# Kernel optimization log

Measured on AMD Instinct MI355X. Metric: run time of the kernel, lower is better.

Reference implementation:

```python
import jax, jax.numpy as jnp
import numpy as np
import math

B, N, E, H = 2, 10000, 160000, 128
ET = 8
EPS = 1e-5


def setup_inputs() -> dict:
    key = jax.random.key(0)
    ks = jax.random.split(key, 20)
    s = 1.0 / math.sqrt(H)
    inp = {
        "hidden": jax.random.normal(ks[0], (B, N, H), jnp.float32),
        "time_emb": jax.random.normal(ks[1], (B, N, H), jnp.float32),
        "edge_index": jax.random.randint(ks[2], (2, E), 0, N),
        "edge_type": jax.random.randint(ks[3], (E,), 0, ET),
        # parameters
        "edge_emb": jax.random.normal(ks[4], (ET, H), jnp.float32),
        "Wq": jax.random.normal(ks[5], (H, H), jnp.float32) * s,
        "bq": jnp.zeros((H,), jnp.float32),
        "Wk": jax.random.normal(ks[6], (H, H), jnp.float32) * s,
        "bk": jnp.zeros((H,), jnp.float32),
        "Wv": jax.random.normal(ks[7], (H, H), jnp.float32) * s,
        "bv": jnp.zeros((H,), jnp.float32),
        "We": jax.random.normal(ks[8], (H, 1), jnp.float32) * s,
        "be": jnp.zeros((1,), jnp.float32),
        "W1": jax.random.normal(ks[9], (3 * H, H), jnp.float32) * (1.0 / math.sqrt(3 * H)),
        "b1": jnp.zeros((H,), jnp.float32),
        "W2": jax.random.normal(ks[10], (H, H), jnp.float32) * s,
        "b2": jnp.zeros((H,), jnp.float32),
        "gamma": jnp.ones((H,), jnp.float32),
        "beta": jnp.zeros((H,), jnp.float32),
    }
    return inp


def _forward(hidden, time_emb, edge_index, edge_type, edge_emb,
             Wq, bq, Wk, bk, Wv, bv, We, be, W1, b1, W2, b2, gamma, beta):
    src, tgt = edge_index[0], edge_index[1]
    # edge-wise gathers: [B, E, H]
    src_h = hidden[:, src]
    tgt_h = hidden[:, tgt]
    src_t = time_emb[:, src]
    tgt_t = time_emb[:, tgt]
    edge_h = edge_emb[edge_type][None, :, :]  # [1, E, H] broadcasts over batch

    query = (tgt_h + tgt_t) @ Wq + bq
    key = (src_h + src_t + edge_h) @ Wk + bk
    value = (src_h + edge_h) @ Wv + bv

    logits = jnp.einsum("beh,beh->be", query, key) / math.sqrt(H)
    logits = logits + (edge_h @ We + be)[..., 0]  # edge bias broadcast over batch

    # segment softmax per target node (equivalent to the per-node masked softmax loop)
    lT = logits.T  # [E, B]
    seg_max = jax.ops.segment_max(lT, tgt, num_segments=N)          # [N, B]
    seg_max = jnp.where(jnp.isfinite(seg_max), seg_max, 0.0)
    ex = jnp.exp(lT - seg_max[tgt])                                  # [E, B]
    seg_sum = jax.ops.segment_sum(ex, tgt, num_segments=N)           # [N, B]
    weights = (ex / seg_sum[tgt]).T                                  # [B, E]

    messages = value * weights[..., None]                            # [B, E, H]
    # scatter-add to target nodes
    agg = jax.ops.segment_sum(jnp.swapaxes(messages, 0, 1), tgt, num_segments=N)  # [N, B, H]
    aggregated = jnp.swapaxes(agg, 0, 1)                             # [B, N, H]

    cat = jnp.concatenate([hidden, aggregated, time_emb], axis=-1)   # [B, N, 3H]
    updated = jax.nn.silu(cat @ W1 + b1) @ W2 + b2

    x = hidden + updated  # dropout p=0 -> identity
    mu = jnp.mean(x, axis=-1, keepdims=True)
    var = jnp.var(x, axis=-1, keepdims=True)
    return (x - mu) * jax.lax.rsqrt(var + EPS) * gamma + beta


def reference(hidden, time_emb, edge_index, edge_type, edge_emb,
              Wq, bq, Wk, bk, Wv, bv, We, be, W1, b1, W2, b2, gamma, beta):
    return _forward(hidden, time_emb, edge_index, edge_type, edge_emb,
                    Wq, bq, Wk, bk, Wv, bv, We, be, W1, b1, W2, b2, gamma, beta)
```

## Files before the change

kernel.cpp:

```cpp
#include <hip/hip_runtime.h>
#include <math.h>

constexpr int B_  = 2;
constexpr int N_  = 10000;
constexpr int E_  = 160000;
constexpr int H_  = 128;
constexpr int ET_ = 8;
constexpr int CAP_ = 64;
constexpr float EPS_ = 1e-5f;
constexpr float RSQH = 0.08838834764831845f;

typedef __bf16 bf16x8 __attribute__((ext_vector_type(8)));
typedef short  short8 __attribute__((ext_vector_type(8)));
typedef float  f32x4  __attribute__((ext_vector_type(4)));
typedef unsigned short u16;

__device__ inline u16 bf16b(float f) {
    return __builtin_bit_cast(u16, (__bf16)f);
}

__device__ inline bf16x8 ldfrag(const u16* __restrict__ W, int kc, int nt, int lane) {
    short8 s = *(const short8*)(W + ((kc * 8 + nt) * 64 + lane) * 8);
    return __builtin_bit_cast(bf16x8, s);
}

__global__ __launch_bounds__(256)
void setup_kernel(const float* __restrict__ W1, const float* __restrict__ W2,
                  const float* __restrict__ Wq, const float* __restrict__ Wk,
                  const float* __restrict__ Wv,
                  u16* __restrict__ W1s, u16* __restrict__ W2s,
                  u16* __restrict__ Wqs, u16* __restrict__ Wks, u16* __restrict__ Wvs,
                  const float* __restrict__ edge_emb,
                  const float* __restrict__ bk, const float* __restrict__ bv,
                  const float* __restrict__ We, const float* __restrict__ be,
                  float* __restrict__ Kt, float* __restrict__ Vt, float* __restrict__ eb,
                  int* __restrict__ count)
{
    const int bid = blockIdx.x, tid = threadIdx.x;
    if (bid < 56) {
        int unit = bid >> 1, half = bid & 1;
        const float* src; u16* dst; int kc;
        if (unit < 12)      { src = W1; dst = W1s; kc = unit; }
        else if (unit < 16) { src = W2; dst = W2s; kc = unit - 12; }
        else if (unit < 20) { src = Wq; dst = Wqs; kc = unit - 16; }
        else if (unit < 24) { src = Wk; dst = Wks; kc = unit - 20; }
        else                { src = Wv; dst = Wvs; kc = unit - 24; }
        int nt = half * 4 + (tid >> 6), lane = tid & 63;
        int q = lane >> 4, c = lane & 15;
        int kbase = kc * 32 + q * 8;
        int col = nt * 16 + c;
        u16* out = dst + ((kc * 8 + nt) * 64 + lane) * 8;
#pragma unroll
        for (int j = 0; j < 8; ++j)
            out[j] = bf16b(src[(kbase + j) * H_ + col]);
    } else if (bid < 64) {
        int t = bid - 56;
        const float* ep = edge_emb + t * H_;
        __shared__ float red[2];
        int j = tid;
        if (j < 128) {
            float ak = bk[j], av = bv[j];
            for (int d = 0; d < H_; d += 4) {
                float e0 = ep[d], e1 = ep[d+1], e2 = ep[d+2], e3 = ep[d+3];
                ak += e0*Wk[(d+0)*H_+j] + e1*Wk[(d+1)*H_+j] + e2*Wk[(d+2)*H_+j] + e3*Wk[(d+3)*H_+j];
                av += e0*Wv[(d+0)*H_+j] + e1*Wv[(d+1)*H_+j] + e2*Wv[(d+2)*H_+j] + e3*Wv[(d+3)*H_+j];
            }
            Kt[t*H_ + j] = ak;
            Vt[t*H_ + j] = av;
            float pe = ep[j] * We[j];
#pragma unroll
            for (int off = 32; off; off >>= 1) pe += __shfl_xor(pe, off);
            if ((j & 63) == 0) red[j >> 6] = pe;
        }
        __syncthreads();
        if (j == 0) eb[t] = red[0] + red[1] + be[0];
    } else {
        int i0 = (bid - 64) * 1024;
        for (int i = i0 + tid; i < i0 + 1024; i += 256)
            if (i < N_) count[i] = 0;
    }
}

__global__ __launch_bounds__(256)
void scatter_qkv_kernel(const int* __restrict__ src, const int* __restrict__ tgt,
                        const int* __restrict__ type, int* __restrict__ count,
                        int* __restrict__ slots,
                        const float* __restrict__ hidden, const float* __restrict__ time_emb,
                        const u16* __restrict__ Wqs, const u16* __restrict__ Wks,
                        const u16* __restrict__ Wvs, const float* __restrict__ bq,
                        u16* __restrict__ Q, u16* __restrict__ KV)
{
    if (blockIdx.x < 625) {
        int e = blockIdx.x * 256 + threadIdx.x;
        if (e < E_) {
            int t = tgt[e];
            int pos = atomicAdd(&count[t], 1);
            slots[t * CAP_ + pos] = src[e] | (type[e] << 16);
        }
        return;
    }
    const int wv = threadIdx.x >> 6, lane = threadIdx.x & 63;
    const int tile = (blockIdx.x - 625) * 4 + wv;
    if (tile >= (B_ * N_) / 16) return;
    const int nbase = tile * 16;
    const int m = lane & 15, q = lane >> 4;
    const int koff = q * 8;

    bf16x8 aq[4], av[4];
    const float* hp = hidden   + (nbase + m) * H_ + koff;
    const float* tp = time_emb + (nbase + m) * H_ + koff;
#pragma unroll
    for (int kc = 0; kc < 4; ++kc) {
        float4 h0 = *(const float4*)(hp + kc * 32);
        float4 h1 = *(const float4*)(hp + kc * 32 + 4);
        float4 t0 = *(const float4*)(tp + kc * 32);
        float4 t1 = *(const float4*)(tp + kc * 32 + 4);
        bf16x8 fv, fq;
        fv[0]=(__bf16)h0.x; fv[1]=(__bf16)h0.y; fv[2]=(__bf16)h0.z; fv[3]=(__bf16)h0.w;
        fv[4]=(__bf16)h1.x; fv[5]=(__bf16)h1.y; fv[6]=(__bf16)h1.z; fv[7]=(__bf16)h1.w;
        fq[0]=(__bf16)(h0.x+t0.x); fq[1]=(__bf16)(h0.y+t0.y);
        fq[2]=(__bf16)(h0.z+t0.z); fq[3]=(__bf16)(h0.w+t0.w);
        fq[4]=(__bf16)(h1.x+t1.x); fq[5]=(__bf16)(h1.y+t1.y);
        fq[6]=(__bf16)(h1.z+t1.z); fq[7]=(__bf16)(h1.w+t1.w);
        av[kc] = fv; aq[kc] = fq;
    }

    f32x4 accq[8], acck[8], accv[8];
#pragma unroll
    for (int nt = 0; nt < 8; ++nt) { accq[nt] = (f32x4)0.f; acck[nt] = (f32x4)0.f; accv[nt] = (f32x4)0.f; }

#pragma unroll
    for (int kc = 0; kc < 4; ++kc) {
#pragma unroll
        for (int nt = 0; nt < 8; ++nt) {
            bf16x8 bfq = ldfrag(Wqs, kc, nt, lane);
            bf16x8 bfk = ldfrag(Wks, kc, nt, lane);
            bf16x8 bfv = ldfrag(Wvs, kc, nt, lane);
            accq[nt] = __builtin_amdgcn_mfma_f32_16x16x32_bf16(aq[kc], bfq, accq[nt], 0, 0, 0);
            acck[nt] = __builtin_amdgcn_mfma_f32_16x16x32_bf16(aq[kc], bfk, acck[nt], 0, 0, 0);
            accv[nt] = __builtin_amdgcn_mfma_f32_16x16x32_bf16(av[kc], bfv, accv[nt], 0, 0, 0);
        }
    }

#pragma unroll
    for (int nt = 0; nt < 8; ++nt) {
        int col = nt * 16 + m;
        float bqc = bq[col];
#pragma unroll
        for (int r = 0; r < 4; ++r) {
            int node = nbase + q * 4 + r;
            Q[(size_t)node * H_ + col] = bf16b(accq[nt][r] + bqc);
            KV[(size_t)node * 256 + col]       = bf16b(acck[nt][r]);
            KV[(size_t)node * 256 + 128 + col] = bf16b(accv[nt][r]);
        }
    }
}

__global__ __launch_bounds__(256)
void attn_kernel(const u16* __restrict__ Qb, const u16* __restrict__ KV,
                 const float* __restrict__ Kt, const float* __restrict__ Vt,
                 const float* __restrict__ eb,
                 const int* __restrict__ count, const int* __restrict__ slots,
                 u16* __restrict__ aggb)
{
    __shared__ float bias_s[4][8];
    __shared__ __align__(16) u16 vt_s[8][128];

    const int tid = threadIdx.x;
    const int wv = tid >> 6, lane = tid & 63;
    const int g = lane >> 4, lam = lane & 15;

    for (int idx = tid; idx < ET_ * H_; idx += 256)
        vt_s[idx >> 7][idx & 127] = bf16b(Vt[idx]);
    __syncthreads();

    const int b = (blockIdx.x >= (N_ / 4)) ? 1 : 0;
    const int n = (blockIdx.x - b * (N_ / 4)) * 4 + wv;
    const int bn = b * N_ + n;
    const int cnt = count[n];
    const int sbase = n * CAP_;
    const u16* __restrict__ KVb = KV + (size_t)(b * N_) * 256;

    int myslot = 0;
    {
        int idx = g + 4 * lam;
        if (idx < cnt) myslot = slots[sbase + idx];
    }
    const int lb = lane & 48;

    float q[8];
    {
        short8 s8 = *(const short8*)(Qb + (size_t)bn * H_ + lam * 8);
        bf16x8 qa = __builtin_bit_cast(bf16x8, s8);
#pragma unroll
        for (int j = 0; j < 8; ++j) q[j] = (float)qa[j];
    }

    {
        const float* k0p = Kt + (2 * g) * H_ + lam * 8;
        const float* k1p = Kt + (2 * g + 1) * H_ + lam * 8;
        float p0 = 0.f, p1 = 0.f;
#pragma unroll
        for (int j = 0; j < 8; ++j) { p0 += q[j] * k0p[j]; p1 += q[j] * k1p[j]; }
#pragma unroll
        for (int msk = 1; msk < 16; msk <<= 1) {
            p0 += __shfl_xor(p0, msk);
            p1 += __shfl_xor(p1, msk);
        }
        if (lam == 0) {
            bias_s[wv][2 * g]     = p0 * RSQH + eb[2 * g];
            bias_s[wv][2 * g + 1] = p1 * RSQH + eb[2 * g + 1];
        }
    }

    float m_g = -INFINITY, l_g = 0.f;
    float acc[8];
#pragma unroll
    for (int j = 0; j < 8; ++j) acc[j] = 0.f;

    int c = g;
    for (; c + 4 < cnt; c += 8) {
        int r = (c - g) >> 2;
        int pk0 = __shfl(myslot, lb + r);
        int pk1 = __shfl(myslot, lb + r + 1);
        int s0 = pk0 & 0xFFFF, t0 = pk0 >> 16;
        int s1 = pk1 & 0xFFFF, t1 = pk1 >> 16;
        short8 k80 = *(const short8*)(KVb + (size_t)s0 * 256 + lam * 8);
        short8 k81 = *(const short8*)(KVb + (size_t)s1 * 256 + lam * 8);
        short8 v80 = *(const short8*)(KVb + (size_t)s0 * 256 + 128 + lam * 8);
        short8 v81 = *(const short8*)(KVb + (size_t)s1 * 256 + 128 + lam * 8);
        short8 vt80 = *(const short8*)(&vt_s[t0][lam * 8]);
        short8 vt81 = *(const short8*)(&vt_s[t1][lam * 8]);
        bf16x8 ka0 = __builtin_bit_cast(bf16x8, k80);
        bf16x8 ka1 = __builtin_bit_cast(bf16x8, k81);
        float p0 = 0.f, p1 = 0.f;
#pragma unroll
        for (int j = 0; j < 8; ++j) {
            p0 += q[j] * (float)ka0[j];
            p1 += q[j] * (float)ka1[j];
        }
#pragma unroll
        for (int msk = 1; msk < 16; msk <<= 1) {
            p0 += __shfl_xor(p0, msk);
            p1 += __shfl_xor(p1, msk);
        }
        float lg0 = p0 * RSQH + bias_s[wv][t0];
        float lg1 = p1 * RSQH + bias_s[wv][t1];
        float mx = fmaxf(lg0, lg1);
        if (mx > m_g + 8.f) {
            float rs = __expf(m_g - mx);
            l_g *= rs;
#pragma unroll
            for (int j = 0; j < 8; ++j) acc[j] *= rs;
            m_g = mx;
        }
        float w0 = __expf(lg0 - m_g);
        float w1 = __expf(lg1 - m_g);
        l_g += w0 + w1;
        bf16x8 va0  = __builtin_bit_cast(bf16x8, v80);
        bf16x8 va1  = __builtin_bit_cast(bf16x8, v81);
        bf16x8 vta0 = __builtin_bit_cast(bf16x8, vt80);
        bf16x8 vta1 = __builtin_bit_cast(bf16x8, vt81);
#pragma unroll
        for (int j = 0; j < 8; ++j)
            acc[j] += w0 * ((float)va0[j] + (float)vta0[j])
                    + w1 * ((float)va1[j] + (float)vta1[j]);
    }
    if (c < cnt) {
        int r = (c - g) >> 2;
        int pk0 = __shfl(myslot, lb + r);
        int s0 = pk0 & 0xFFFF, t0 = pk0 >> 16;
        short8 k80 = *(const short8*)(KVb + (size_t)s0 * 256 + lam * 8);
        short8 v80 = *(const short8*)(KVb + (size_t)s0 * 256 + 128 + lam * 8);
        short8 vt80 = *(const short8*)(&vt_s[t0][lam * 8]);
        bf16x8 ka0 = __builtin_bit_cast(bf16x8, k80);
        float p0 = 0.f;
#pragma unroll
        for (int j = 0; j < 8; ++j) p0 += q[j] * (float)ka0[j];
#pragma unroll
        for (int msk = 1; msk < 16; msk <<= 1) p0 += __shfl_xor(p0, msk);
        float lg0 = p0 * RSQH + bias_s[wv][t0];
        if (lg0 > m_g + 8.f) {
            float rs = __expf(m_g - lg0);
            l_g *= rs;
#pragma unroll
            for (int j = 0; j < 8; ++j) acc[j] *= rs;
            m_g = lg0;
        }
        float w0 = __expf(lg0 - m_g);
        l_g += w0;
        bf16x8 va0  = __builtin_bit_cast(bf16x8, v80);
        bf16x8 vta0 = __builtin_bit_cast(bf16x8, vt80);
#pragma unroll
        for (int j = 0; j < 8; ++j)
            acc[j] += w0 * ((float)va0[j] + (float)vta0[j]);
    }

    float M = fmaxf(m_g, __shfl_xor(m_g, 16));
    M = fmaxf(M, __shfl_xor(M, 32));
    float rs = (m_g == M) ? 1.f : __expf(m_g - M);
    l_g *= rs;
#pragma unroll
    for (int j = 0; j < 8; ++j) {
        acc[j] *= rs;
        acc[j] += __shfl_xor(acc[j], 16);
        acc[j] += __shfl_xor(acc[j], 32);
    }
    l_g += __shfl_xor(l_g, 16);
    l_g += __shfl_xor(l_g, 32);

    if (g == 0) {
        float invL = (cnt > 0) ? 1.f / l_g : 0.f;
        bf16x8 o;
#pragma unroll
        for (int j = 0; j < 8; ++j) o[j] = (__bf16)(acc[j] * invL);
        *(short8*)(aggb + (size_t)bn * H_ + lam * 8) = __builtin_bit_cast(short8, o);
    }
}

__global__ __launch_bounds__(256)
void mlp_mfma_kernel(const float* __restrict__ hidden, const u16* __restrict__ aggb,
                     const float* __restrict__ time_emb,
                     const u16* __restrict__ W1s, const u16* __restrict__ W2s,
                     const float* __restrict__ b1, const float* __restrict__ b2,
                     const float* __restrict__ gamma, const float* __restrict__ beta,
                     float* __restrict__ out)
{
    __shared__ __align__(16) u16 h1s[4][16][136];
    const int wv = threadIdx.x >> 6, lane = threadIdx.x & 63;
    const int tile = blockIdx.x * 4 + wv;
    if (tile >= (B_ * N_) / 16) return;
    const int nbase = tile * 16;
    const int m = lane & 15, q = lane >> 4;
    const int koff = q * 8;

    bf16x8 a[12];
    const float* hp = hidden   + (nbase + m) * H_ + koff;
    const float* tp = time_emb + (nbase + m) * H_ + koff;
    const u16*   ap = aggb + (size_t)(nbase + m) * H_ + koff;
#pragma unroll
    for (int kc = 0; kc < 4; ++kc) {
        float4 h0 = *(const float4*)(hp + kc * 32);
        float4 h1 = *(const float4*)(hp + kc * 32 + 4);
        float4 t0 = *(const float4*)(tp + kc * 32);
        float4 t1 = *(const float4*)(tp + kc * 32 + 4);
        bf16x8 fh, ft;
        fh[0]=(__bf16)h0.x; fh[1]=(__bf16)h0.y; fh[2]=(__bf16)h0.z; fh[3]=(__bf16)h0.w;
        fh[4]=(__bf16)h1.x; fh[5]=(__bf16)h1.y; fh[6]=(__bf16)h1.z; fh[7]=(__bf16)h1.w;
        ft[0]=(__bf16)t0.x; ft[1]=(__bf16)t0.y; ft[2]=(__bf16)t0.z; ft[3]=(__bf16)t0.w;
        ft[4]=(__bf16)t1.x; ft[5]=(__bf16)t1.y; ft[6]=(__bf16)t1.z; ft[7]=(__bf16)t1.w;
        a[0 * 4 + kc] = fh;
        a[2 * 4 + kc] = ft;
        short8 s8 = *(const short8*)(ap + kc * 32);
        a[1 * 4 + kc] = __builtin_bit_cast(bf16x8, s8);
    }

    f32x4 acc[8];
#pragma unroll
    for (int nt = 0; nt < 8; ++nt) acc[nt] = (f32x4)0.f;
#pragma unroll
    for (int kc = 0; kc < 12; ++kc) {
#pragma unroll
        for (int nt = 0; nt < 8; ++nt) {
            bf16x8 bf = ldfrag(W1s, kc, nt, lane);
            acc[nt] = __builtin_amdgcn_mfma_f32_16x16x32_bf16(a[kc], bf, acc[nt], 0, 0, 0);
        }
    }

#pragma unroll
    for (int nt = 0; nt < 8; ++nt) {
        int col = nt * 16 + m;
        float bb = b1[col];
#pragma unroll
        for (int r = 0; r < 4; ++r) {
            float v = acc[nt][r] + bb;
            float h = v / (1.f + __expf(-v));
            h1s[wv][q * 4 + r][col] = bf16b(h);
        }
    }

    f32x4 acc2[8];
#pragma unroll
    for (int nt = 0; nt < 8; ++nt) acc2[nt] = (f32x4)0.f;
#pragma unroll
    for (int kc = 0; kc < 4; ++kc) {
        short8 s8 = *(const short8*)&h1s[wv][m][kc * 32 + koff];
        bf16x8 a2 = __builtin_bit_cast(bf16x8, s8);
#pragma unroll
        for (int nt = 0; nt < 8; ++nt) {
            bf16x8 bf = ldfrag(W2s, kc, nt, lane);
            acc2[nt] = __builtin_amdgcn_mfma_f32_16x16x32_bf16(a2, bf, acc2[nt], 0, 0, 0);
        }
    }

    float x[8][4];
#pragma unroll
    for (int nt = 0; nt < 8; ++nt) {
        int col = nt * 16 + m;
        float bb = b2[col];
#pragma unroll
        for (int r = 0; r < 4; ++r) {
            int node = nbase + q * 4 + r;
            x[nt][r] = hidden[node * H_ + col] + acc2[nt][r] + bb;
        }
    }
#pragma unroll
    for (int r = 0; r < 4; ++r) {
        float s = 0.f, ss = 0.f;
#pragma unroll
        for (int nt = 0; nt < 8; ++nt) { s += x[nt][r]; ss += x[nt][r] * x[nt][r]; }
#pragma unroll
        for (int off = 1; off < 16; off <<= 1) {
            s  += __shfl_xor(s, off);
            ss += __shfl_xor(ss, off);
        }
        float mu  = s * (1.f / H_);
        float var = ss * (1.f / H_) - mu * mu;
        float rs  = rsqrtf(var + EPS_);
        int node = nbase + q * 4 + r;
#pragma unroll
        for (int nt = 0; nt < 8; ++nt) {
            int col = nt * 16 + m;
            out[node * H_ + col] = (x[nt][r] - mu) * rs * gamma[col] + beta[col];
        }
    }
}

extern "C" void kernel_launch(void* const* d_in, const int* in_sizes, int n_in,
                              void* d_out, int out_size, void* d_ws, size_t ws_size,
                              hipStream_t stream)
{
    const float* hidden   = (const float*)d_in[0];
    const float* time_emb = (const float*)d_in[1];
    const int*   eidx     = (const int*)d_in[2];
    const int*   etype    = (const int*)d_in[3];
    const float* edge_emb = (const float*)d_in[4];
    const float* Wq = (const float*)d_in[5];
    const float* bq = (const float*)d_in[6];
    const float* Wk = (const float*)d_in[7];
    const float* bk = (const float*)d_in[8];
    const float* Wv = (const float*)d_in[9];
    const float* bv = (const float*)d_in[10];
    const float* We = (const float*)d_in[11];
    const float* be = (const float*)d_in[12];
    const float* W1 = (const float*)d_in[13];
    const float* b1 = (const float*)d_in[14];
    const float* W2 = (const float*)d_in[15];
    const float* b2 = (const float*)d_in[16];
    const float* gamma = (const float*)d_in[17];
    const float* beta  = (const float*)d_in[18];
    float* out = (float*)d_out;

    constexpr int BNH = B_ * N_ * H_;
    u16* Qb   = (u16*)d_ws;
    u16* KVb  = Qb + BNH;
    u16* aggb = KVb + (size_t)B_ * N_ * 256;
    float* Kt  = (float*)(aggb + BNH);
    float* Vt  = Kt + ET_ * H_;
    float* ebt = Vt + ET_ * H_;
    int* count = (int*)(ebt + ET_);
    int* slots = count + N_;
    uintptr_t wp = (uintptr_t)(slots + N_ * CAP_);
    wp = (wp + 15) & ~(uintptr_t)15;
    u16* W1s = (u16*)wp;
    u16* W2s = W1s + 384 * 128;
    u16* Wqs = W2s + 128 * 128;
    u16* Wks = Wqs + 128 * 128;
    u16* Wvs = Wks + 128 * 128;

    const int* esrc = eidx;
    const int* etgt = eidx + E_;

    setup_kernel<<<74, 256, 0, stream>>>(
        W1, W2, Wq, Wk, Wv, W1s, W2s, Wqs, Wks, Wvs,
        edge_emb, bk, bv, We, be, Kt, Vt, ebt, count);
    scatter_qkv_kernel<<<625 + 313, 256, 0, stream>>>(
        esrc, etgt, etype, count, slots,
        hidden, time_emb, Wqs, Wks, Wvs, bq, Qb, KVb);
    attn_kernel<<<(B_ * N_) / 4, 256, 0, stream>>>(
        Qb, KVb, Kt, Vt, ebt, count, slots, aggb);
    mlp_mfma_kernel<<<313, 256, 0, stream>>>(
        hidden, aggb, time_emb, W1s, W2s, b1, b2, gamma, beta, out);
}
```

Measured before the change: 173.2 us.

## Process both batch elements per wavefront in attention kernel

The attention kernel now handles both batch entries for a target node in one wavefront, so the grid is halved. Slot lookups, edge-type table reads, the per-type bias setup and the loop control are shared across the two batches, and twice as many independent K/V loads are in flight per iteration. The cost is roughly double the accumulator registers per lane and fewer blocks, which could lower occupancy and the latency hiding that comes with it.

```diff
diff --git a/kernel.cpp b/kernel.cpp
--- a/kernel.cpp
+++ b/kernel.cpp
@@ -163,7 +163,7 @@
                  const int* __restrict__ count, const int* __restrict__ slots,
                  u16* __restrict__ aggb)
 {
-    __shared__ float bias_s[4][8];
+    __shared__ float bias_s[4][2][8];
     __shared__ __align__(16) u16 vt_s[8][128];
 
     const int tid = threadIdx.x;
@@ -174,12 +174,11 @@
         vt_s[idx >> 7][idx & 127] = bf16b(Vt[idx]);
     __syncthreads();
 
-    const int b = (blockIdx.x >= (N_ / 4)) ? 1 : 0;
-    const int n = (blockIdx.x - b * (N_ / 4)) * 4 + wv;
-    const int bn = b * N_ + n;
+    const int n = blockIdx.x * 4 + wv;
     const int cnt = count[n];
     const int sbase = n * CAP_;
-    const u16* __restrict__ KVb = KV + (size_t)(b * N_) * 256;
+    const u16* __restrict__ KV0 = KV;
+    const u16* __restrict__ KV1 = KV + (size_t)N_ * 256;
 
     int myslot = 0;
     {
@@ -188,133 +187,220 @@
     }
     const int lb = lane & 48;
 
-    float q[8];
+    float q0[8], q1[8];
     {
-        short8 s8 = *(const short8*)(Qb + (size_t)bn * H_ + lam * 8);
-        bf16x8 qa = __builtin_bit_cast(bf16x8, s8);
-#pragma unroll
-        for (int j = 0; j < 8; ++j) q[j] = (float)qa[j];
+        short8 sa = *(const short8*)(Qb + (size_t)n * H_ + lam * 8);
+        short8 sb = *(const short8*)(Qb + (size_t)(N_ + n) * H_ + lam * 8);
+        bf16x8 qa = __builtin_bit_cast(bf16x8, sa);
+        bf16x8 qb = __builtin_bit_cast(bf16x8, sb);
+#pragma unroll
+        for (int j = 0; j < 8; ++j) { q0[j] = (float)qa[j]; q1[j] = (float)qb[j]; }
     }
 
     {
         const float* k0p = Kt + (2 * g) * H_ + lam * 8;
         const float* k1p = Kt + (2 * g + 1) * H_ + lam * 8;
-        float p0 = 0.f, p1 = 0.f;
-#pragma unroll
-        for (int j = 0; j < 8; ++j) { p0 += q[j] * k0p[j]; p1 += q[j] * k1p[j]; }
+        float p00 = 0.f, p01 = 0.f, p10 = 0.f, p11 = 0.f;
+#pragma unroll
+        for (int j = 0; j < 8; ++j) {
+            float ka = k0p[j], kb = k1p[j];
+            p00 += q0[j] * ka; p01 += q0[j] * kb;
+            p10 += q1[j] * ka; p11 += q1[j] * kb;
+        }
 #pragma unroll
         for (int msk = 1; msk < 16; msk <<= 1) {
-            p0 += __shfl_xor(p0, msk);
-            p1 += __shfl_xor(p1, msk);
+            p00 += __shfl_xor(p00, msk);
+            p01 += __shfl_xor(p01, msk);
+            p10 += __shfl_xor(p10, msk);
+            p11 += __shfl_xor(p11, msk);
         }
         if (lam == 0) {
-            bias_s[wv][2 * g]     = p0 * RSQH + eb[2 * g];
-            bias_s[wv][2 * g + 1] = p1 * RSQH + eb[2 * g + 1];
-        }
-    }
-
-    float m_g = -INFINITY, l_g = 0.f;
-    float acc[8];
-#pragma unroll
-    for (int j = 0; j < 8; ++j) acc[j] = 0.f;
+            bias_s[wv][0][2 * g]     = p00 * RSQH + eb[2 * g];
+            bias_s[wv][0][2 * g + 1] = p01 * RSQH + eb[2 * g + 1];
+            bias_s[wv][1][2 * g]     = p10 * RSQH + eb[2 * g];
+            bias_s[wv][1][2 * g + 1] = p11 * RSQH + eb[2 * g + 1];
+        }
+    }
+
+    float m0 = -INFINITY, l0 = 0.f, m1 = -INFINITY, l1 = 0.f;
+    float acc0[8], acc1[8];
+#pragma unroll
+    for (int j = 0; j < 8; ++j) { acc0[j] = 0.f; acc1[j] = 0.f; }
 
     int c = g;
     for (; c + 4 < cnt; c += 8) {
         int r = (c - g) >> 2;
-        int pk0 = __shfl(myslot, lb + r);
-        int pk1 = __shfl(myslot, lb + r + 1);
-        int s0 = pk0 & 0xFFFF, t0 = pk0 >> 16;
-        int s1 = pk1 & 0xFFFF, t1 = pk1 >> 16;
-        short8 k80 = *(const short8*)(KVb + (size_t)s0 * 256 + lam * 8);
-        short8 k81 = *(const short8*)(KVb + (size_t)s1 * 256 + lam * 8);
-        short8 v80 = *(const short8*)(KVb + (size_t)s0 * 256 + 128 + lam * 8);
-        short8 v81 = *(const short8*)(KVb + (size_t)s1 * 256 + 128 + lam * 8);
-        short8 vt80 = *(const short8*)(&vt_s[t0][lam * 8]);
-        short8 vt81 = *(const short8*)(&vt_s[t1][lam * 8]);
-        bf16x8 ka0 = __builtin_bit_cast(bf16x8, k80);
-        bf16x8 ka1 = __builtin_bit_cast(bf16x8, k81);
-        float p0 = 0.f, p1 = 0.f;
+        int pkA = __shfl(myslot, lb + r);
+        int pkB = __shfl(myslot, lb + r + 1);
+        int sA = pkA & 0xFFFF, tA = pkA >> 16;
+        int sB = pkB & 0xFFFF, tB = pkB >> 16;
+        short8 k0A = *(const short8*)(KV0 + (size_t)sA * 256 + lam * 8);
+        short8 k0B = *(const short8*)(KV0 + (size_t)sB * 256 + lam * 8);
+        short8 k1A = *(const short8*)(KV1 + (size_t)sA * 256 + lam * 8);
+        short8 k1B = *(const short8*)(KV1 + (size_t)sB * 256 + lam * 8);
+        short8 v0A = *(const short8*)(KV0 + (size_t)sA * 256 + 128 + lam * 8);
+        short8 v0B = *(const short8*)(KV0 + (size_t)sB * 256 + 128 + lam * 8);
+        short8 v1A = *(const short8*)(KV1 + (size_t)sA * 256 + 128 + lam * 8);
+        short8 v1B = *(const short8*)(KV1 + (size_t)sB * 256 + 128 + lam * 8);
+        short8 vtA = *(const short8*)(&vt_s[tA][lam * 8]);
+        short8 vtB = *(const short8*)(&vt_s[tB][lam * 8]);
+        bf16x8 ka0A = __builtin_bit_cast(bf16x8, k0A);
+        bf16x8 ka0B = __builtin_bit_cast(bf16x8, k0B);
+        bf16x8 ka1A = __builtin_bit_cast(bf16x8, k1A);
+        bf16x8 ka1B = __builtin_bit_cast(bf16x8, k1B);
+        float d0A = 0.f, d0B = 0.f, d1A = 0.f, d1B = 0.f;
 #pragma unroll
         for (int j = 0; j < 8; ++j) {
-            p0 += q[j] * (float)ka0[j];
-            p1 += q[j] * (float)ka1[j];
+            d0A += q0[j] * (float)ka0A[j];
+            d0B += q0[j] * (float)ka0B[j];
+            d1A += q1[j] * (float)ka1A[j];
+            d1B += q1[j] * (float)ka1B[j];
         }
 #pragma unroll
         for (int msk = 1; msk < 16; msk <<= 1) {
-            p0 += __shfl_xor(p0, msk);
-            p1 += __shfl_xor(p1, msk);
-        }
-        float lg0 = p0 * RSQH + bias_s[wv][t0];
-        float lg1 = p1 * RSQH + bias_s[wv][t1];
-        float mx = fmaxf(lg0, lg1);
-        if (mx > m_g + 8.f) {
-            float rs = __expf(m_g - mx);
-            l_g *= rs;
-#pragma unroll
-            for (int j = 0; j < 8; ++j) acc[j] *= rs;
-            m_g = mx;
-        }
-        float w0 = __expf(lg0 - m_g);
-        float w1 = __expf(lg1 - m_g);
-        l_g += w0 + w1;
-        bf16x8 va0  = __builtin_bit_cast(bf16x8, v80);
-        bf16x8 va1  = __builtin_bit_cast(bf16x8, v81);
-        bf16x8 vta0 = __builtin_bit_cast(bf16x8, vt80);
-        bf16x8 vta1 = __builtin_bit_cast(bf16x8, vt81);
-#pragma unroll
-        for (int j = 0; j < 8; ++j)
-            acc[j] += w0 * ((float)va0[j] + (float)vta0[j])
-                    + w1 * ((float)va1[j] + (float)vta1[j]);
+            d0A += __shfl_xor(d0A, msk);
+            d0B += __shfl_xor(d0B, msk);
+            d1A += __shfl_xor(d1A, msk);
+            d1B += __shfl_xor(d1B, msk);
+        }
+        float lg0A = d0A * RSQH + bias_s[wv][0][tA];
+        float lg0B = d0B * RSQH + bias_s[wv][0][tB];
+        float lg1A = d1A * RSQH + bias_s[wv][1][tA];
+        float lg1B = d1B * RSQH + bias_s[wv][1][tB];
+        bf16x8 va0A = __builtin_bit_cast(bf16x8, v0A);
+        bf16x8 va0B = __builtin_bit_cast(bf16x8, v0B);
+        bf16x8 va1A = __builtin_bit_cast(bf16x8, v1A);
+        bf16x8 va1B = __builtin_bit_cast(bf16x8, v1B);
+        bf16x8 vtaA = __builtin_bit_cast(bf16x8, vtA);
+        bf16x8 vtaB = __builtin_bit_cast(bf16x8, vtB);
+        {
+            float mx = fmaxf(lg0A, lg0B);
+            if (mx > m0 + 8.f) {
+                float rs = __expf(m0 - mx);
+                l0 *= rs;
+#pragma unroll
+                for (int j = 0; j < 8; ++j) acc0[j] *= rs;
+                m0 = mx;
+            }
+            float wA = __expf(lg0A - m0);
+            float wB = __expf(lg0B - m0);
+            l0 += wA + wB;
+#pragma unroll
+            for (int j = 0; j < 8; ++j)
+                acc0[j] += wA * ((float)va0A[j] + (float)vtaA[j])
+                         + wB * ((float)va0B[j] + (float)vtaB[j]);
+        }
+        {
+            float mx = fmaxf(lg1A, lg1B);
+            if (mx > m1 + 8.f) {
+                float rs = __expf(m1 - mx);
+                l1 *= rs;
+#pragma unroll
+                for (int j = 0; j < 8; ++j) acc1[j] *= rs;
+                m1 = mx;
+            }
+            float wA = __expf(lg1A - m1);
+            float wB = __expf(lg1B - m1);
+            l1 += wA + wB;
+#pragma unroll
+            for (int j = 0; j < 8; ++j)
+                acc1[j] += wA * ((float)va1A[j] + (float)vtaA[j])
+                         + wB * ((float)va1B[j] + (float)vtaB[j]);
+        }
     }
     if (c < cnt) {
         int r = (c - g) >> 2;
-        int pk0 = __shfl(myslot, lb + r);
-        int s0 = pk0 & 0xFFFF, t0 = pk0 >> 16;
-        short8 k80 = *(const short8*)(KVb + (size_t)s0 * 256 + lam * 8);
-        short8 v80 = *(const short8*)(KVb + (size_t)s0 * 256 + 128 + lam * 8);
-        short8 vt80 = *(const short8*)(&vt_s[t0][lam * 8]);
-        bf16x8 ka0 = __builtin_bit_cast(bf16x8, k80);
-        float p0 = 0.f;
-#pragma unroll
-        for (int j = 0; j < 8; ++j) p0 += q[j] * (float)ka0[j];
-#pragma unroll
-        for (int msk = 1; msk < 16; msk <<= 1) p0 += __shfl_xor(p0, msk);
-        float lg0 = p0 * RSQH + bias_s[wv][t0];
-        if (lg0 > m_g + 8.f) {
-            float rs = __expf(m_g - lg0);
-            l_g *= rs;
-#pragma unroll
-            for (int j = 0; j < 8; ++j) acc[j] *= rs;
-            m_g = lg0;
-        }
-        float w0 = __expf(lg0 - m_g);
-        l_g += w0;
-        bf16x8 va0  = __builtin_bit_cast(bf16x8, v80);
-        bf16x8 vta0 = __builtin_bit_cast(bf16x8, vt80);
+        int pkA = __shfl(myslot, lb + r);
+        int sA = pkA & 0xFFFF, tA = pkA >> 16;
+        short8 k0A = *(const short8*)(KV0 + (size_t)sA * 256 + lam * 8);
+        short8 k1A = *(const short8*)(KV1 + (size_t)sA * 256 + lam * 8);
+        short8 v0A = *(const short8*)(KV0 + (size_t)sA * 256 + 128 + lam * 8);
+        short8 v1A = *(const short8*)(KV1 + (size_t)sA * 256 + 128 + lam * 8);
+        short8 vtA = *(const short8*)(&vt_s[tA][lam * 8]);
+        bf16x8 ka0A = __builtin_bit_cast(bf16x8, k0A);
+        bf16x8 ka1A = __builtin_bit_cast(bf16x8, k1A);
+        float d0A = 0.f, d1A = 0.f;
+#pragma unroll
+        for (int j = 0; j < 8; ++j) {
+            d0A += q0[j] * (float)ka0A[j];
+            d1A += q1[j] * (float)ka1A[j];
+        }
+#pragma unroll
+        for (int msk = 1; msk < 16; msk <<= 1) {
+            d0A += __shfl_xor(d0A, msk);
+            d1A += __shfl_xor(d1A, msk);
+        }
+        float lg0A = d0A * RSQH + bias_s[wv][0][tA];
+        float lg1A = d1A * RSQH + bias_s[wv][1][tA];
+        bf16x8 va0A = __builtin_bit_cast(bf16x8, v0A);
+        bf16x8 va1A = __builtin_bit_cast(bf16x8, v1A);
+        bf16x8 vtaA = __builtin_bit_cast(bf16x8, vtA);
+        if (lg0A > m0 + 8.f) {
+            float rs = __expf(m0 - lg0A);
+            l0 *= rs;
+#pragma unroll
+            for (int j = 0; j < 8; ++j) acc0[j] *= rs;
+            m0 = lg0A;
+        }
+        float w0 = __expf(lg0A - m0);
+        l0 += w0;
 #pragma unroll
         for (int j = 0; j < 8; ++j)
-            acc[j] += w0 * ((float)va0[j] + (float)vta0[j]);
-    }
-
-    float M = fmaxf(m_g, __shfl_xor(m_g, 16));
-    M = fmaxf(M, __shfl_xor(M, 32));
-    float rs = (m_g == M) ? 1.f : __expf(m_g - M);
-    l_g *= rs;
-#pragma unroll
-    for (int j = 0; j < 8; ++j) {
-        acc[j] *= rs;
-        acc[j] += __shfl_xor(acc[j], 16);
-        acc[j] += __shfl_xor(acc[j], 32);
-    }
-    l_g += __shfl_xor(l_g, 16);
-    l_g += __shfl_xor(l_g, 32);
+            acc0[j] += w0 * ((float)va0A[j] + (float)vtaA[j]);
+        if (lg1A > m1 + 8.f) {
+            float rs = __expf(m1 - lg1A);
+            l1 *= rs;
+#pragma unroll
+            for (int j = 0; j < 8; ++j) acc1[j] *= rs;
+            m1 = lg1A;
+        }
+        float w1 = __expf(lg1A - m1);
+        l1 += w1;
+#pragma unroll
+        for (int j = 0; j < 8; ++j)
+            acc1[j] += w1 * ((float)va1A[j] + (float)vtaA[j]);
+    }
+
+    {
+        float M = fmaxf(m0, __shfl_xor(m0, 16));
+        M = fmaxf(M, __shfl_xor(M, 32));
+        float rs = (m0 == M) ? 1.f : __expf(m0 - M);
+        l0 *= rs;
+#pragma unroll
+        for (int j = 0; j < 8; ++j) {
+            acc0[j] *= rs;
+            acc0[j] += __shfl_xor(acc0[j], 16);
+            acc0[j] += __shfl_xor(acc0[j], 32);
+        }
+        l0 += __shfl_xor(l0, 16);
+        l0 += __shfl_xor(l0, 32);
+    }
+    {
+        float M = fmaxf(m1, __shfl_xor(m1, 16));
+        M = fmaxf(M, __shfl_xor(M, 32));
+        float rs = (m1 == M) ? 1.f : __expf(m1 - M);
+        l1 *= rs;
+#pragma unroll
+        for (int j = 0; j < 8; ++j) {
+            acc1[j] *= rs;
+            acc1[j] += __shfl_xor(acc1[j], 16);
+            acc1[j] += __shfl_xor(acc1[j], 32);
+        }
+        l1 += __shfl_xor(l1, 16);
+        l1 += __shfl_xor(l1, 32);
+    }
 
     if (g == 0) {
-        float invL = (cnt > 0) ? 1.f / l_g : 0.f;
-        bf16x8 o;
-#pragma unroll
-        for (int j = 0; j < 8; ++j) o[j] = (__bf16)(acc[j] * invL);
-        *(short8*)(aggb + (size_t)bn * H_ + lam * 8) = __builtin_bit_cast(short8, o);
+        float invL0 = (cnt > 0) ? 1.f / l0 : 0.f;
+        float invL1 = (cnt > 0) ? 1.f / l1 : 0.f;
+        bf16x8 o0, o1;
+#pragma unroll
+        for (int j = 0; j < 8; ++j) {
+            o0[j] = (__bf16)(acc0[j] * invL0);
+            o1[j] = (__bf16)(acc1[j] * invL1);
+        }
+        *(short8*)(aggb + (size_t)n * H_ + lam * 8)        = __builtin_bit_cast(short8, o0);
+        *(short8*)(aggb + (size_t)(N_ + n) * H_ + lam * 8) = __builtin_bit_cast(short8, o1);
     }
 }
 
@@ -477,7 +563,7 @@
     scatter_qkv_kernel<<<625 + 313, 256, 0, stream>>>(
         esrc, etgt, etype, count, slots,
         hidden, time_emb, Wqs, Wks, Wvs, bq, Qb, KVb);
-    attn_kernel<<<(B_ * N_) / 4, 256, 0, stream>>>(
+    attn_kernel<<<N_ / 4, 256, 0, stream>>>(
         Qb, KVb, Kt, Vt, ebt, count, slots, aggb);
     mlp_mfma_kernel<<<313, 256, 0, stream>>>(
         hidden, aggb, time_emb, W1s, W2s, b1, b2, gamma, beta, out);
```

Measured after the change: 173.7 us. About the same (+0.3%).

## Split output columns across wave pairs in QKV and MLP kernels

Applied to the files above, without the earlier changes.

Each 16-node tile is now handled by two waves, each computing half of the output columns, in both the QKV projection and the fused MLP/LayerNorm kernel. Grid sizes double, so more waves are spread across the GPU's compute units for these small GEMMs. In the MLP kernel the two halves share the SiLU intermediate and the LayerNorm partial sums through shared memory, which needs block-wide barriers. The cost is duplicated input loading and bf16 conversion per tile, plus the synchronisation overhead.

```diff
diff --git a/kernel.cpp b/kernel.cpp
--- a/kernel.cpp
+++ b/kernel.cpp
@@ -100,8 +100,8 @@
         return;
     }
     const int wv = threadIdx.x >> 6, lane = threadIdx.x & 63;
-    const int tile = (blockIdx.x - 625) * 4 + wv;
-    if (tile >= (B_ * N_) / 16) return;
+    const int tile = (blockIdx.x - 625) * 2 + (wv >> 1);
+    const int hf = wv & 1;
     const int nbase = tile * 16;
     const int m = lane & 15, q = lane >> 4;
     const int koff = q * 8;
@@ -125,17 +125,18 @@
         av[kc] = fv; aq[kc] = fq;
     }
 
-    f32x4 accq[8], acck[8], accv[8];
-#pragma unroll
-    for (int nt = 0; nt < 8; ++nt) { accq[nt] = (f32x4)0.f; acck[nt] = (f32x4)0.f; accv[nt] = (f32x4)0.f; }
+    f32x4 accq[4], acck[4], accv[4];
+#pragma unroll
+    for (int nt = 0; nt < 4; ++nt) { accq[nt] = (f32x4)0.f; acck[nt] = (f32x4)0.f; accv[nt] = (f32x4)0.f; }
 
 #pragma unroll
     for (int kc = 0; kc < 4; ++kc) {
 #pragma unroll
-        for (int nt = 0; nt < 8; ++nt) {
-            bf16x8 bfq = ldfrag(Wqs, kc, nt, lane);
-            bf16x8 bfk = ldfrag(Wks, kc, nt, lane);
-            bf16x8 bfv = ldfrag(Wvs, kc, nt, lane);
+        for (int nt = 0; nt < 4; ++nt) {
+            int ntg = hf * 4 + nt;
+            bf16x8 bfq = ldfrag(Wqs, kc, ntg, lane);
+            bf16x8 bfk = ldfrag(Wks, kc, ntg, lane);
+            bf16x8 bfv = ldfrag(Wvs, kc, ntg, lane);
             accq[nt] = __builtin_amdgcn_mfma_f32_16x16x32_bf16(aq[kc], bfq, accq[nt], 0, 0, 0);
             acck[nt] = __builtin_amdgcn_mfma_f32_16x16x32_bf16(aq[kc], bfk, acck[nt], 0, 0, 0);
             accv[nt] = __builtin_amdgcn_mfma_f32_16x16x32_bf16(av[kc], bfv, accv[nt], 0, 0, 0);
@@ -143,8 +144,8 @@
     }
 
 #pragma unroll
-    for (int nt = 0; nt < 8; ++nt) {
-        int col = nt * 16 + m;
+    for (int nt = 0; nt < 4; ++nt) {
+        int col = (hf * 4 + nt) * 16 + m;
         float bqc = bq[col];
 #pragma unroll
         for (int r = 0; r < 4; ++r) {
@@ -326,17 +327,19 @@
                      const float* __restrict__ gamma, const float* __restrict__ beta,
                      float* __restrict__ out)
 {
-    __shared__ __align__(16) u16 h1s[4][16][136];
+    __shared__ __align__(16) u16 h1s[2][16][136];
+    __shared__ float sp[2][16][2], ssp[2][16][2];
     const int wv = threadIdx.x >> 6, lane = threadIdx.x & 63;
-    const int tile = blockIdx.x * 4 + wv;
-    if (tile >= (B_ * N_) / 16) return;
+    const int p  = wv >> 1;
+    const int hf = wv & 1;
+    const int tile = blockIdx.x * 2 + p;
     const int nbase = tile * 16;
     const int m = lane & 15, q = lane >> 4;
     const int koff = q * 8;
 
     bf16x8 a[12];
-    const float* hp = hidden   + (nbase + m) * H_ + koff;
-    const float* tp = time_emb + (nbase + m) * H_ + koff;
+    const float* hp = hidden   + (size_t)(nbase + m) * H_ + koff;
+    const float* tp = time_emb + (size_t)(nbase + m) * H_ + koff;
     const u16*   ap = aggb + (size_t)(nbase + m) * H_ + koff;
 #pragma unroll
     for (int kc = 0; kc < 4; ++kc) {
@@ -355,73 +358,82 @@
         a[1 * 4 + kc] = __builtin_bit_cast(bf16x8, s8);
     }
 
-    f32x4 acc[8];
-#pragma unroll
-    for (int nt = 0; nt < 8; ++nt) acc[nt] = (f32x4)0.f;
+    f32x4 acc1[4];
+#pragma unroll
+    for (int nt = 0; nt < 4; ++nt) acc1[nt] = (f32x4)0.f;
 #pragma unroll
     for (int kc = 0; kc < 12; ++kc) {
 #pragma unroll
-        for (int nt = 0; nt < 8; ++nt) {
-            bf16x8 bf = ldfrag(W1s, kc, nt, lane);
-            acc[nt] = __builtin_amdgcn_mfma_f32_16x16x32_bf16(a[kc], bf, acc[nt], 0, 0, 0);
-        }
-    }
-
-#pragma unroll
-    for (int nt = 0; nt < 8; ++nt) {
-        int col = nt * 16 + m;
+        for (int nt = 0; nt < 4; ++nt) {
+            bf16x8 bf = ldfrag(W1s, kc, hf * 4 + nt, lane);
+            acc1[nt] = __builtin_amdgcn_mfma_f32_16x16x32_bf16(a[kc], bf, acc1[nt], 0, 0, 0);
+        }
+    }
+#pragma unroll
+    for (int nt = 0; nt < 4; ++nt) {
+        int col = (hf * 4 + nt) * 16 + m;
         float bb = b1[col];
 #pragma unroll
         for (int r = 0; r < 4; ++r) {
-            float v = acc[nt][r] + bb;
+            float v = acc1[nt][r] + bb;
             float h = v / (1.f + __expf(-v));
-            h1s[wv][q * 4 + r][col] = bf16b(h);
-        }
-    }
-
-    f32x4 acc2[8];
-#pragma unroll
-    for (int nt = 0; nt < 8; ++nt) acc2[nt] = (f32x4)0.f;
+            h1s[p][q * 4 + r][col] = bf16b(h);
+        }
+    }
+    __syncthreads();
+
+    f32x4 acc2[4];
+#pragma unroll
+    for (int nt = 0; nt < 4; ++nt) acc2[nt] = (f32x4)0.f;
 #pragma unroll
     for (int kc = 0; kc < 4; ++kc) {
-        short8 s8 = *(const short8*)&h1s[wv][m][kc * 32 + koff];
+        short8 s8 = *(const short8*)(&h1s[p][m][kc * 32 + koff]);
         bf16x8 a2 = __builtin_bit_cast(bf16x8, s8);
 #pragma unroll
-        for (int nt = 0; nt < 8; ++nt) {
-            bf16x8 bf = ldfrag(W2s, kc, nt, lane);
+        for (int nt = 0; nt < 4; ++nt) {
+            bf16x8 bf = ldfrag(W2s, kc, hf * 4 + nt, lane);
             acc2[nt] = __builtin_amdgcn_mfma_f32_16x16x32_bf16(a2, bf, acc2[nt], 0, 0, 0);
         }
     }
 
-    float x[8][4];
-#pragma unroll
-    for (int nt = 0; nt < 8; ++nt) {
-        int col = nt * 16 + m;
+    float x[4][4];
+#pragma unroll
+    for (int nt = 0; nt < 4; ++nt) {
+        int col = (hf * 4 + nt) * 16 + m;
         float bb = b2[col];
 #pragma unroll
         for (int r = 0; r < 4; ++r) {
             int node = nbase + q * 4 + r;
-            x[nt][r] = hidden[node * H_ + col] + acc2[nt][r] + bb;
+            x[nt][r] = hidden[(size_t)node * H_ + col] + acc2[nt][r] + bb;
         }
     }
 #pragma unroll
     for (int r = 0; r < 4; ++r) {
-        float s = 0.f, ss = 0.f;
-#pragma unroll
-        for (int nt = 0; nt < 8; ++nt) { s += x[nt][r]; ss += x[nt][r] * x[nt][r]; }
+        float s  = (x[0][r] + x[1][r]) + (x[2][r] + x[3][r]);
+        float ss = (x[0][r] * x[0][r] + x[1][r] * x[1][r])
+                 + (x[2][r] * x[2][r] + x[3][r] * x[3][r]);
 #pragma unroll
         for (int off = 1; off < 16; off <<= 1) {
             s  += __shfl_xor(s, off);
             ss += __shfl_xor(ss, off);
         }
+        if (m == 0) { sp[p][q * 4 + r][hf] = s; ssp[p][q * 4 + r][hf] = ss; }
+    }
+    __syncthreads();
+
+#pragma unroll
+    for (int r = 0; r < 4; ++r) {
+        int nl = q * 4 + r;
+        float s  = sp[p][nl][0]  + sp[p][nl][1];
+        float ss = ssp[p][nl][0] + ssp[p][nl][1];
         float mu  = s * (1.f / H_);
         float var = ss * (1.f / H_) - mu * mu;
-        float rs  = rsqrtf(var + EPS_);
-        int node = nbase + q * 4 + r;
-#pragma unroll
-        for (int nt = 0; nt < 8; ++nt) {
-            int col = nt * 16 + m;
-            out[node * H_ + col] = (x[nt][r] - mu) * rs * gamma[col] + beta[col];
+        float rsn = rsqrtf(var + EPS_);
+        int node = nbase + nl;
+#pragma unroll
+        for (int nt = 0; nt < 4; ++nt) {
+            int col = (hf * 4 + nt) * 16 + m;
+            out[(size_t)node * H_ + col] = (x[nt][r] - mu) * rsn * gamma[col] + beta[col];
         }
     }
 }
@@ -474,11 +486,11 @@
     setup_kernel<<<74, 256, 0, stream>>>(
         W1, W2, Wq, Wk, Wv, W1s, W2s, Wqs, Wks, Wvs,
         edge_emb, bk, bv, We, be, Kt, Vt, ebt, count);
-    scatter_qkv_kernel<<<625 + 313, 256, 0, stream>>>(
+    scatter_qkv_kernel<<<625 + 625, 256, 0, stream>>>(
         esrc, etgt, etype, count, slots,
         hidden, time_emb, Wqs, Wks, Wvs, bq, Qb, KVb);
     attn_kernel<<<(B_ * N_) / 4, 256, 0, stream>>>(
         Qb, KVb, Kt, Vt, ebt, count, slots, aggb);
-    mlp_mfma_kernel<<<313, 256, 0, stream>>>(
+    mlp_mfma_kernel<<<625, 256, 0, stream>>>(
         hidden, aggb, time_emb, W1s, W2s, b1, b2, gamma, beta, out);
 }
```

New measurement: 173.9 us. About the same (+0.4%).
